# Optimization experiments

Hardware: AMD Instinct MI355X
Metric: run time of the kernel (lower is better)

The kernel has to match this reference:

```python
import jax, jax.numpy as jnp
import numpy as np

D_MODEL, D_STATE, EXPAND, HEADDIM = 768, 64, 2, 64
D_INNER = EXPAND * D_MODEL            # 1536
NHEADS = D_INNER // HEADDIM           # 24
D_IN_PROJ = 2 * D_INNER + 2 * D_STATE + 2 * NHEADS  # 3248
DT_MIN, DT_MAX, DT_INIT_FLOOR, A_FLOOR = 1e-3, 1e-1, 1e-4, 1e-4
LN_EPS = 1e-5


def setup_inputs() -> dict:
    key = jax.random.key(0)
    ks = jax.random.split(key, 8)
    B, L = 2, 1024
    u = jax.random.normal(ks[0], (B, L, D_MODEL), dtype=jnp.float32)
    s_in = 1.0 / np.sqrt(D_MODEL)
    s_out = 1.0 / np.sqrt(D_INNER)
    Win = jax.random.uniform(ks[1], (D_IN_PROJ, D_MODEL), jnp.float32, -s_in, s_in)
    Wout = jax.random.uniform(ks[2], (D_MODEL, D_INNER), jnp.float32, -s_out, s_out)
    _dt = jnp.clip(jnp.exp(jax.random.uniform(ks[3], (NHEADS,)) * (np.log(DT_MAX) - np.log(DT_MIN)) + np.log(DT_MIN)), DT_INIT_FLOOR, None)
    dt_bias = _dt + jnp.log(-jnp.expm1(-_dt))
    D = jnp.ones((NHEADS,), jnp.float32)
    Bg = jnp.ones((D_STATE,), jnp.float32)
    Bb = jnp.zeros((D_STATE,), jnp.float32)
    Cg = jnp.ones((D_STATE,), jnp.float32)
    Cb = jnp.zeros((D_STATE,), jnp.float32)
    return {"u": u, "Win": Win, "Wout": Wout, "dt_bias": dt_bias, "D": D,
            "Bg": Bg, "Bb": Bb, "Cg": Cg, "Cb": Cb}


def _layernorm(x, g, b):
    m = jnp.mean(x, axis=-1, keepdims=True)
    v = jnp.var(x, axis=-1, keepdims=True)
    return (x - m) * jax.lax.rsqrt(v + LN_EPS) * g + b


def reference(u, Win, Wout, dt_bias, D, Bg, Bb, Cg, Cb):
    B_, L, _ = u.shape
    nH, hD, dS = NHEADS, HEADDIM, D_STATE
    proj = u @ Win.T  # (B, L, D_IN_PROJ)
    z, x, Bp, Cp, dd_dt, dd_A = jnp.split(
        proj, np.cumsum([D_INNER, D_INNER, dS, dS, nH])[:-0 or None], axis=-1) if False else (
        proj[..., :D_INNER],
        proj[..., D_INNER:2 * D_INNER],
        proj[..., 2 * D_INNER:2 * D_INNER + dS],
        proj[..., 2 * D_INNER + dS:2 * D_INNER + 2 * dS],
        proj[..., 2 * D_INNER + 2 * dS:2 * D_INNER + 2 * dS + nH],
        proj[..., 2 * D_INNER + 2 * dS + nH:])
    x = x.reshape(B_, L, nH, hD)
    z = z.reshape(B_, L, nH, hD)
    Bn = _layernorm(Bp, Bg, Bb)  # (B, L, dS), shared across heads
    Cn = _layernorm(Cp, Cg, Cb)
    DT = jax.nn.softplus(dd_dt + dt_bias)                    # (B, L, nH)
    A = jnp.minimum(-jax.nn.softplus(dd_A), -A_FLOOR)        # (B, L, nH)
    dec = jnp.exp(A * DT)                                    # (B, L, nH)

    def step(h, inp):
        x_t, Bn_t, Cn_t, DT_t, dec_t = inp
        upd = jnp.einsum('bhp,bn->bhpn', x_t, Bn_t) * DT_t[..., None, None]
        h = dec_t[..., None, None] * h + upd
        y_t = jnp.einsum('bhpn,bn->bhp', h, Cn_t) + D[None, :, None] * x_t
        return h, y_t

    h0 = jnp.zeros((B_, nH, hD, dS), u.dtype)
    xs = (jnp.swapaxes(x, 0, 1), jnp.swapaxes(Bn, 0, 1), jnp.swapaxes(Cn, 0, 1),
          jnp.swapaxes(DT, 0, 1), jnp.swapaxes(dec, 0, 1))
    _, ys = jax.lax.scan(step, h0, xs)            # ys: (L, B, nH, hD)
    y = jnp.swapaxes(ys, 0, 1) * jax.nn.silu(z)   # (B, L, nH, hD)
    y = y.reshape(B_, L, D_INNER)
    return y @ Wout.T
```

## Files before the change

### kernel.cpp

```cpp
#include <hip/hip_runtime.h>
#include <cstdint>

#define D_MODEL   768
#define D_STATE   64
#define D_INNER   1536
#define NHEADS    24
#define HEADDIM   64
#define D_PROJ    3248
#define BATCH     2
#define SEQ       1024
#define ROWS      (BATCH*SEQ)
#define LN_EPS    1e-5f
#define A_FLOOR   1e-4f
#define QC        64
#define NCH       (SEQ/QC)
#define LSTR      72

#define RG_U    32
#define RG_WIN  52
#define RG_WO   12
#define KT_1    24
#define KT_2    48

typedef __attribute__((ext_vector_type(8))) short short8;
typedef __attribute__((ext_vector_type(4))) float f32x4;

__device__ __forceinline__ unsigned short f2bf(float f) {
  union { float f; uint32_t u; } v; v.f = f;
  uint32_t r = (v.u + 0x7FFFu + ((v.u >> 16) & 1u)) >> 16;
  return (unsigned short)r;
}
__device__ __forceinline__ float bf2f(unsigned short u) {
  union { uint32_t u; float f; } v; v.u = (uint32_t)u << 16;
  return v.f;
}
__device__ __forceinline__ void storeC(float v, float* p) { *p = v; }
__device__ __forceinline__ void storeC(float v, unsigned short* p) { *p = f2bf(v); }

__device__ __forceinline__ void gload_lds16(const void* g, void* l) {
  __builtin_amdgcn_global_load_lds(
      (const __attribute__((address_space(1))) unsigned int*)g,
      (__attribute__((address_space(3))) unsigned int*)l, 16, 0, 0);
}

template <int N>
__device__ __forceinline__ void wait_vm() {
  static_assert(N == 0 || N == 2 || N == 3 || N == 4 || N == 6 || N == 8,
                "unsupported vmcnt");
  if constexpr (N == 0) asm volatile("s_waitcnt vmcnt(0)" ::: "memory");
  else if constexpr (N == 2) asm volatile("s_waitcnt vmcnt(2)" ::: "memory");
  else if constexpr (N == 3) asm volatile("s_waitcnt vmcnt(3)" ::: "memory");
  else if constexpr (N == 4) asm volatile("s_waitcnt vmcnt(4)" ::: "memory");
  else if constexpr (N == 6) asm volatile("s_waitcnt vmcnt(6)" ::: "memory");
  else if constexpr (N == 8) asm volatile("s_waitcnt vmcnt(8)" ::: "memory");
}

__global__ __launch_bounds__(256) void pack_all_kernel(
    const float* __restrict__ u, const float* __restrict__ Win,
    const float* __restrict__ Wout, unsigned short* __restrict__ upk,
    unsigned short* __restrict__ Winpk, unsigned short* __restrict__ Wopk) {
  int b = blockIdx.x;
  const float* src; unsigned short* dst; int K, RG, kt, rg, srcRows;
  if (b < KT_1 * RG_U) {
    src = u; dst = upk; K = 768; RG = RG_U; kt = b / RG_U; rg = b % RG_U; srcRows = ROWS;
  } else if (b < KT_1 * RG_U + KT_1 * RG_WIN) {
    int i = b - KT_1 * RG_U;
    src = Win; dst = Winpk; K = 768; RG = RG_WIN; kt = i / RG_WIN; rg = i % RG_WIN; srcRows = D_PROJ;
  } else {
    int i = b - KT_1 * RG_U - KT_1 * RG_WIN;
    src = Wout; dst = Wopk; K = 1536; RG = RG_WO; kt = i / RG_WO; rg = i % RG_WO; srcRows = D_MODEL;
  }
  const int t = threadIdx.x;
  const int lr = t >> 2, cq = t & 3;
  const int R = rg * 64 + lr;
  float4 v0 = make_float4(0.f, 0.f, 0.f, 0.f), v1 = v0;
  if (R < srcRows) {
    const float* p = src + (size_t)R * K + kt * 32 + cq * 8;
    v0 = *(const float4*)p;
    v1 = *(const float4*)(p + 4);
  }
  ushort4 oa, ob;
  oa.x = f2bf(v0.x); oa.y = f2bf(v0.y); oa.z = f2bf(v0.z); oa.w = f2bf(v0.w);
  ob.x = f2bf(v1.x); ob.y = f2bf(v1.y); ob.z = f2bf(v1.z); ob.w = f2bf(v1.w);
  unsigned short* o = dst + ((size_t)(kt * RG + rg) * 4 + cq) * 512 + lr * 8;
  *(ushort4*)o = oa;
  *(ushort4*)(o + 4) = ob;
}

template <int TBM, int TBN, int GX, int GY, bool XMAJOR, typename CT>
__global__ __launch_bounds__(256) void gemm_bt_bf16(
    const unsigned short* __restrict__ A, const unsigned short* __restrict__ B,
    CT* __restrict__ C, int aRG, int bRG, int M, int N, int K) {
  constexpr int MF = TBM / 32;
  constexpr int NF = TBN / 32;
  constexpr int NSA = TBM / 16;
  constexpr int NSB = TBN / 16;
  constexpr int LPW = (NSA + NSB) / 4;
  static_assert((NSA + NSB) % 4 == 0, "segments must split evenly over waves");
  constexpr int NWG = GX * GY;
  constexpr int PER = NWG / 8;
  static_assert(NWG % 8 == 0, "grid must split evenly over 8 XCDs");
  __shared__ unsigned short Asm[4][TBM * 32];
  __shared__ unsigned short Bsm[4][TBN * 32];

  const int tid = threadIdx.x;
  const int wv = tid >> 6, lane = tid & 63;
  const int kTiles = K >> 5;

  const int sk = blockIdx.y;
  A += (size_t)sk * kTiles * aRG * 2048;
  B += (size_t)sk * kTiles * bRG * 2048;
  C += (size_t)sk * M * N;

  const int g = (blockIdx.x & 7) * PER + (blockIdx.x >> 3);
  int bx, by;
  if constexpr (XMAJOR) { by = g / GX; bx = g - by * GX; }
  else                  { bx = g / GY; by = g - bx * GY; }
  const int bm = by * TBM, bn = bx * TBN;

  const int wm = (wv & 1) * (TBM / 2);
  const int wn = (wv >> 1) * (TBN / 2);
  const int gq = lane >> 4, r = lane & 15;

  f32x4 acc[MF][NF];
#pragma unroll
  for (int i = 0; i < MF; ++i)
#pragma unroll
    for (int j = 0; j < NF; ++j) acc[i][j] = (f32x4){0.f, 0.f, 0.f, 0.f};

  auto stage = [&](int kt, int buf) {
    for (int s = wv; s < NSA + NSB; s += 4) {
      if (s < NSA) {
        const unsigned short* src =
            A + ((size_t)kt * aRG + (bm >> 6) + (s >> 2)) * 2048 + (s & 3) * 512 + lane * 8;
        gload_lds16(src, (void*)(&Asm[buf][s * 512]));
      } else {
        int s2 = s - NSA;
        const unsigned short* src =
            B + ((size_t)kt * bRG + (bn >> 6) + (s2 >> 2)) * 2048 + (s2 & 3) * 512 + lane * 8;
        gload_lds16(src, (void*)(&Bsm[buf][s2 * 512]));
      }
    }
  };

  stage(0, 0);
  stage(1, 1);
  stage(2, 2);

  for (int t = 0; t < kTiles; ++t) {
    const int cur = t & 3;
    if (t + 2 < kTiles)      wait_vm<2 * LPW>();
    else if (t + 1 < kTiles) wait_vm<LPW>();
    else                     wait_vm<0>();
    __builtin_amdgcn_s_barrier();
    asm volatile("" ::: "memory");

    if (t + 3 < kTiles) stage(t + 3, (t + 3) & 3);

    short8 a[MF], b[NF];
#pragma unroll
    for (int mf = 0; mf < MF; ++mf) {
      int ra = wm + mf * 16 + r;
      a[mf] = *(const short8*)&Asm[cur][(ra >> 6) * 2048 + gq * 512 + (ra & 63) * 8];
    }
#pragma unroll
    for (int nf = 0; nf < NF; ++nf) {
      int rb = wn + nf * 16 + r;
      b[nf] = *(const short8*)&Bsm[cur][(rb >> 6) * 2048 + gq * 512 + (rb & 63) * 8];
    }
#pragma unroll
    for (int mf = 0; mf < MF; ++mf)
#pragma unroll
      for (int nf = 0; nf < NF; ++nf)
        acc[mf][nf] = __builtin_amdgcn_mfma_f32_16x16x32_bf16(a[mf], b[nf], acc[mf][nf], 0, 0, 0);
  }

#pragma unroll
  for (int mf = 0; mf < MF; ++mf) {
#pragma unroll
    for (int nf = 0; nf < NF; ++nf) {
      int col = bn + wn + nf * 16 + r;
      if (col < N) {
#pragma unroll
        for (int q = 0; q < 4; ++q) {
          int row = bm + wm + mf * 16 + gq * 4 + q;
          storeC(acc[mf][nf][q], &C[(size_t)row * N + col]);
        }
      }
    }
  }
}

__global__ __launch_bounds__(256) void reduce2_kernel(
    const float* __restrict__ P, float* __restrict__ out, int n4) {
  int i = blockIdx.x * 256 + threadIdx.x;
  if (i < n4) {
    float4 a = *(const float4*)(P + (size_t)i * 4);
    float4 b = *(const float4*)(P + (size_t)(n4 + i) * 4);
    a.x += b.x; a.y += b.y; a.z += b.z; a.w += b.w;
    *(float4*)(out + (size_t)i * 4) = a;
  }
}

__device__ __forceinline__ float softplusf(float x) {
  return (x > 20.f) ? x : log1pf(expf(x));
}
__device__ __forceinline__ float wave_sum64(float v) {
#pragma unroll
  for (int o = 32; o > 0; o >>= 1) v += __shfl_xor(v, o);
  return v;
}

__global__ __launch_bounds__(256) void prep_kernel(
    const unsigned short* __restrict__ proj, const float* __restrict__ dt_bias,
    const float* __restrict__ Bg, const float* __restrict__ Bb,
    const float* __restrict__ Cg, const float* __restrict__ Cb,
    unsigned short* __restrict__ BC, float2* __restrict__ aDT) {
  const int r = blockIdx.x * 4 + (threadIdx.x >> 6);
  const int lane = threadIdx.x & 63;
  const unsigned short* p = proj + (size_t)r * D_PROJ;

  float bp = bf2f(p[2 * D_INNER + lane]);
  float cp = bf2f(p[2 * D_INNER + D_STATE + lane]);

  float mb = wave_sum64(bp) * (1.f / 64.f);
  float mc = wave_sum64(cp) * (1.f / 64.f);
  float db = bp - mb, dc = cp - mc;
  float vb = wave_sum64(db * db) * (1.f / 64.f);
  float vc = wave_sum64(dc * dc) * (1.f / 64.f);
  float bn = db * rsqrtf(vb + LN_EPS) * Bg[lane] + Bb[lane];
  float cn = dc * rsqrtf(vc + LN_EPS) * Cg[lane] + Cb[lane];
  BC[(size_t)r * 128 + lane]      = f2bf(bn);
  BC[(size_t)r * 128 + 64 + lane] = f2bf(cn);

  if (lane < NHEADS) {
    float ddt = bf2f(p[2 * D_INNER + 2 * D_STATE + lane]);
    float dA  = bf2f(p[2 * D_INNER + 2 * D_STATE + NHEADS + lane]);
    float DT = softplusf(ddt + dt_bias[lane]);
    float Aa = fminf(-softplusf(dA), -A_FLOOR);
    int b = r >> 10;
    int t = r & 1023;
    aDT[((size_t)(b * NHEADS + lane) << 10) + t] = make_float2(Aa * DT, DT);
  }
}

__device__ __forceinline__ float wave_prefix_incl(float v, int lane) {
#pragma unroll
  for (int o = 1; o < 64; o <<= 1) {
    float w = __shfl_up(v, o);
    if (lane >= o) v += w;
  }
  return v;
}

__global__ __launch_bounds__(256) void chunk_state_kernel(
    const unsigned short* __restrict__ proj, const unsigned short* __restrict__ BC,
    const float2* __restrict__ aDT, float* __restrict__ Tbuf,
    float* __restrict__ Ebuf) {
  const int blk = blockIdx.x;
  const int c = blk & (NCH - 1), bh = blk >> 4;
  const int b = bh / NHEADS, hh = bh % NHEADS;
  const int tid = threadIdx.x;

  __shared__ unsigned short BT[64 * LSTR];
  __shared__ unsigned short XT[64 * LSTR];
  __shared__ float coeff[QC];
  __shared__ float etot[1];

  if (tid < 64) {
    float2 ad = aDT[((size_t)bh << 10) + c * QC + tid];
    float cs = wave_prefix_incl(ad.x, tid);
    float tot = __shfl(cs, 63);
    coeff[tid] = ad.y * __expf(tot - cs);
    if (tid == 63) etot[0] = __expf(tot);
  }
  __syncthreads();

  for (int i = tid; i < 1024; i += 256) {
    int s = i >> 4;
    int q = (i & 15) * 4;
    int r = b * SEQ + c * QC + s;
    ushort4 bv = *(const ushort4*)(BC + (size_t)r * 128 + q);
    ushort4 xv = *(const ushort4*)(proj + (size_t)r * D_PROJ + D_INNER + hh * 64 + q);
    float cf = coeff[s];
    BT[(q + 0) * LSTR + s] = bv.x;
    BT[(q + 1) * LSTR + s] = bv.y;
    BT[(q + 2) * LSTR + s] = bv.z;
    BT[(q + 3) * LSTR + s] = bv.w;
    XT[(q + 0) * LSTR + s] = f2bf(bf2f(xv.x) * cf);
    XT[(q + 1) * LSTR + s] = f2bf(bf2f(xv.y) * cf);
    XT[(q + 2) * LSTR + s] = f2bf(bf2f(xv.z) * cf);
    XT[(q + 3) * LSTR + s] = f2bf(bf2f(xv.w) * cf);
  }
  __syncthreads();

  const int w = tid >> 6, l = tid & 63;
  const int r16 = l & 15, g = l >> 4;
  f32x4 acc[4];
#pragma unroll
  for (int i = 0; i < 4; ++i) acc[i] = (f32x4){0.f, 0.f, 0.f, 0.f};

#pragma unroll
  for (int kk = 0; kk < 2; ++kk) {
    short8 a = *(const short8*)&BT[(w * 16 + r16) * LSTR + kk * 32 + g * 8];
#pragma unroll
    for (int pf = 0; pf < 4; ++pf) {
      short8 bf = *(const short8*)&XT[(pf * 16 + r16) * LSTR + kk * 32 + g * 8];
      acc[pf] = __builtin_amdgcn_mfma_f32_16x16x32_bf16(a, bf, acc[pf], 0, 0, 0);
    }
  }

  float* T = Tbuf + (size_t)blk * 4096;
#pragma unroll
  for (int pf = 0; pf < 4; ++pf)
#pragma unroll
    for (int q = 0; q < 4; ++q)
      T[(size_t)(w * 16 + g * 4 + q) * 64 + pf * 16 + r16] = acc[pf][q];
  if (tid == 0) Ebuf[blk] = etot[0];
}

__global__ __launch_bounds__(256) void interchunk_kernel(
    const float* __restrict__ Tbuf, const float* __restrict__ Ebuf,
    float* __restrict__ Sinbuf) {
  const int bh = blockIdx.x >> 2, part = blockIdx.x & 3;
  const int tid = threadIdx.x;
  const size_t eo = (size_t)part * 1024 + tid * 4;
  float4 s = make_float4(0.f, 0.f, 0.f, 0.f);
#pragma unroll
  for (int c = 0; c < NCH; ++c) {
    size_t off = ((size_t)(bh * NCH + c)) * 4096 + eo;
    *(float4*)(Sinbuf + off) = s;
    float E = Ebuf[bh * NCH + c];
    float4 t4 = *(const float4*)(Tbuf + off);
    s.x = fmaf(E, s.x, t4.x);
    s.y = fmaf(E, s.y, t4.y);
    s.z = fmaf(E, s.z, t4.z);
    s.w = fmaf(E, s.w, t4.w);
  }
}

__global__ __launch_bounds__(256) void chunk_output_kernel(
    const unsigned short* __restrict__ proj, const unsigned short* __restrict__ BC,
    const float2* __restrict__ aDT, const float* __restrict__ Sinbuf,
    const float* __restrict__ Dv, unsigned short* __restrict__ Ybf) {
  const int blk = blockIdx.x;
  const int c = blk & (NCH - 1), bh = blk >> 4;
  const int b = bh / NHEADS, hh = bh % NHEADS;
  const int tid = threadIdx.x;

  __shared__ unsigned short Cc[64 * LSTR];
  __shared__ unsigned short Bc[64 * LSTR];
  __shared__ unsigned short SinT[64 * LSTR];
  __shared__ unsigned short XT[64 * LSTR];
  __shared__ unsigned short Wl[64 * LSTR];
  __shared__ float csum[QC];
  __shared__ float DTs[QC];

  if (tid < 64) {
    float2 ad = aDT[((size_t)bh << 10) + c * QC + tid];
    csum[tid] = wave_prefix_incl(ad.x, tid);
    DTs[tid] = ad.y;
  }

  const size_t sin_base = (size_t)blk * 4096;
  for (int i = tid; i < 1024; i += 256) {
    int s = i >> 4;
    int q = (i & 15) * 4;
    int r = b * SEQ + c * QC + s;
    ushort4 bv = *(const ushort4*)(BC + (size_t)r * 128 + q);
    ushort4 cv = *(const ushort4*)(BC + (size_t)r * 128 + 64 + q);
    ushort4 xv = *(const ushort4*)(proj + (size_t)r * D_PROJ + D_INNER + hh * 64 + q);
    float4 sv = *(const float4*)(Sinbuf + sin_base + (size_t)s * 64 + q);
    *(ushort4*)&Cc[s * LSTR + q] = cv;
    *(ushort4*)&Bc[s * LSTR + q] = bv;
    XT[(q + 0) * LSTR + s] = xv.x;
    XT[(q + 1) * LSTR + s] = xv.y;
    XT[(q + 2) * LSTR + s] = xv.z;
    XT[(q + 3) * LSTR + s] = xv.w;
    SinT[(q + 0) * LSTR + s] = f2bf(sv.x);
    SinT[(q + 1) * LSTR + s] = f2bf(sv.y);
    SinT[(q + 2) * LSTR + s] = f2bf(sv.z);
    SinT[(q + 3) * LSTR + s] = f2bf(sv.w);
  }
  __syncthreads();

  const int w = tid >> 6, l = tid & 63;
  const int r16 = l & 15, g = l >> 4;

  f32x4 accg[4], accy[4];
#pragma unroll
  for (int i = 0; i < 4; ++i) {
    accg[i] = (f32x4){0.f, 0.f, 0.f, 0.f};
    accy[i] = (f32x4){0.f, 0.f, 0.f, 0.f};
  }

#pragma unroll
  for (int kk = 0; kk < 2; ++kk) {
    short8 a = *(const short8*)&Cc[(w * 16 + r16) * LSTR + kk * 32 + g * 8];
#pragma unroll
    for (int f = 0; f < 4; ++f) {
      short8 bf = *(const short8*)&Bc[(f * 16 + r16) * LSTR + kk * 32 + g * 8];
      accg[f] = __builtin_amdgcn_mfma_f32_16x16x32_bf16(a, bf, accg[f], 0, 0, 0);
    }
#pragma unroll
    for (int f = 0; f < 4; ++f) {
      short8 bf = *(const short8*)&SinT[(f * 16 + r16) * LSTR + kk * 32 + g * 8];
      accy[f] = __builtin_amdgcn_mfma_f32_16x16x32_bf16(a, bf, accy[f], 0, 0, 0);
    }
  }

  float cst[4], dsc[4];
#pragma unroll
  for (int q = 0; q < 4; ++q) {
    cst[q] = csum[w * 16 + g * 4 + q];
    dsc[q] = __expf(cst[q]);
  }
#pragma unroll
  for (int sf = 0; sf < 4; ++sf) {
    int s = sf * 16 + r16;
    float cs_s = csum[s], dt_s = DTs[s];
#pragma unroll
    for (int q = 0; q < 4; ++q) {
      int t = w * 16 + g * 4 + q;
      float wv = (s <= t) ? accg[sf][q] * __expf(cst[q] - cs_s) * dt_s : 0.f;
      Wl[t * LSTR + s] = f2bf(wv);
    }
  }
#pragma unroll
  for (int f = 0; f < 4; ++f)
#pragma unroll
    for (int q = 0; q < 4; ++q) accy[f][q] *= dsc[q];
  __syncthreads();

#pragma unroll
  for (int kk = 0; kk < 2; ++kk) {
    short8 a = *(const short8*)&Wl[(w * 16 + r16) * LSTR + kk * 32 + g * 8];
#pragma unroll
    for (int f = 0; f < 4; ++f) {
      short8 bf = *(const short8*)&XT[(f * 16 + r16) * LSTR + kk * 32 + g * 8];
      accy[f] = __builtin_amdgcn_mfma_f32_16x16x32_bf16(a, bf, accy[f], 0, 0, 0);
    }
  }

  const float Dh = Dv[hh];
  const int rg = b * 16 + c;
#pragma unroll
  for (int pf = 0; pf < 4; ++pf) {
    int p = pf * 16 + r16;
    int col = hh * 64 + p;
    int kt = col >> 5;
    int cseg = (col >> 3) & 3;
    int jj = p & 7;
    size_t base = ((size_t)(kt * RG_U + rg) * 4 + cseg) * 512 + jj;
#pragma unroll
    for (int q = 0; q < 4; ++q) {
      int t = w * 16 + g * 4 + q;
      int rr = b * SEQ + c * QC + t;
      float x = bf2f(proj[(size_t)rr * D_PROJ + D_INNER + hh * 64 + p]);
      float z = bf2f(proj[(size_t)rr * D_PROJ + hh * 64 + p]);
      float y = accy[pf][q] + Dh * x;
      Ybf[base + (size_t)t * 8] = f2bf(y * (z / (1.f + __expf(-z))));
    }
  }
}

extern "C" void kernel_launch(void* const* d_in, const int* in_sizes, int n_in,
                              void* d_out, int out_size, void* d_ws, size_t ws_size,
                              hipStream_t stream) {
  const float* u       = (const float*)d_in[0];
  const float* Win     = (const float*)d_in[1];
  const float* Wout    = (const float*)d_in[2];
  const float* dt_bias = (const float*)d_in[3];
  const float* Dv      = (const float*)d_in[4];
  const float* Bg      = (const float*)d_in[5];
  const float* Bb      = (const float*)d_in[6];
  const float* Cg      = (const float*)d_in[7];
  const float* Cb      = (const float*)d_in[8];
  float* out = (float*)d_out;

  float* ws = (float*)d_ws;
  unsigned short* projsh = (unsigned short*)ws;
  float*  after_proj = ws + (size_t)ROWS * D_PROJ / 2;
  unsigned short* BCsh = (unsigned short*)after_proj;
  float*  aDTf    = after_proj + (size_t)ROWS * 128 / 2;
  float2* aDT     = (float2*)aDTf;
  float*  Tbuf    = aDTf + (size_t)2 * BATCH * NHEADS * SEQ;
  float*  Ebuf    = Tbuf + (size_t)BATCH * NHEADS * NCH * 4096;
  float*  Sinbuf  = Ebuf + 1024;
  float*  Woutbff = Sinbuf + (size_t)BATCH * NHEADS * NCH * 4096;
  float*  Pbuf    = Woutbff + 589824;

  unsigned short* upk   = (unsigned short*)Sinbuf;
  unsigned short* Winpk = (unsigned short*)Tbuf;
  unsigned short* Ypk   = (unsigned short*)Tbuf;
  unsigned short* Wopk  = (unsigned short*)Woutbff;

  pack_all_kernel<<<KT_1 * RG_U + KT_1 * RG_WIN + KT_2 * RG_WO, 256, 0, stream>>>(
      u, Win, Wout, upk, Winpk, Wopk);

  gemm_bt_bf16<128, 128, 26, 16, false><<<416, 256, 0, stream>>>(
      upk, Winpk, projsh, RG_U, RG_WIN, ROWS, D_PROJ, D_MODEL);

  prep_kernel<<<ROWS / 4, 256, 0, stream>>>(projsh, dt_bias, Bg, Bb, Cg, Cb, BCsh, aDT);

  chunk_state_kernel<<<BATCH * NHEADS * NCH, 256, 0, stream>>>(projsh, BCsh, aDT, Tbuf, Ebuf);
  interchunk_kernel<<<BATCH * NHEADS * 4, 256, 0, stream>>>(Tbuf, Ebuf, Sinbuf);
  chunk_output_kernel<<<BATCH * NHEADS * NCH, 256, 0, stream>>>(projsh, BCsh, aDT, Sinbuf, Dv, Ypk);

  gemm_bt_bf16<64, 64, 12, 32, true><<<dim3(384, 2), 256, 0, stream>>>(
      Ypk, Wopk, Pbuf, RG_U, RG_WO, ROWS, D_MODEL, D_INNER / 2);
  reduce2_kernel<<<1536, 256, 0, stream>>>(Pbuf, out, ROWS * D_MODEL / 4);
}
```

Baseline: 81.42 us.

## Replace split-K grid and reduce kernel with intra-block K split via LDS reduction

The output GEMM previously ran split-K across a second grid dimension, wrote fp32 partials to a workspace, and summed them in a separate reduce kernel. Now each block has 512 threads; the two groups of four waves each process half of K in separate LDS buffers and combine partials through LDS before storing directly to the output. The pipeline depth also drops from four to three stage buffers to fit the doubled LDS footprint. This removes one kernel launch and a round trip of the partial buffer through global memory, at the cost of halving block count and larger per-block LDS use.

```diff
diff --git a/kernel.cpp b/kernel.cpp
--- a/kernel.cpp
+++ b/kernel.cpp
@@ -87,8 +87,8 @@
   *(ushort4*)(o + 4) = ob;
 }
 
-template <int TBM, int TBN, int GX, int GY, bool XMAJOR, typename CT>
-__global__ __launch_bounds__(256) void gemm_bt_bf16(
+template <int TBM, int TBN, int GX, int GY, bool XMAJOR, int SPLIT, typename CT>
+__global__ __launch_bounds__(256 * SPLIT) void gemm_bt_bf16(
     const unsigned short* __restrict__ A, const unsigned short* __restrict__ B,
     CT* __restrict__ C, int aRG, int bRG, int M, int N, int K) {
   constexpr int MF = TBM / 32;
@@ -100,17 +100,15 @@
   constexpr int NWG = GX * GY;
   constexpr int PER = NWG / 8;
   static_assert(NWG % 8 == 0, "grid must split evenly over 8 XCDs");
-  __shared__ unsigned short Asm[4][TBM * 32];
-  __shared__ unsigned short Bsm[4][TBN * 32];
+  __shared__ unsigned short Asm[SPLIT][3][TBM * 32];
+  __shared__ unsigned short Bsm[SPLIT][3][TBN * 32];
 
   const int tid = threadIdx.x;
-  const int wv = tid >> 6, lane = tid & 63;
-  const int kTiles = K >> 5;
-
-  const int sk = blockIdx.y;
-  A += (size_t)sk * kTiles * aRG * 2048;
-  B += (size_t)sk * kTiles * bRG * 2048;
-  C += (size_t)sk * M * N;
+  const int w = tid >> 6, lane = tid & 63;
+  const int khalf = w >> 2;
+  const int wv = w & 3;
+  const int kTiles = (K / SPLIT) >> 5;
+  const int ktBase = khalf * kTiles;
 
   const int g = (blockIdx.x & 7) * PER + (blockIdx.x >> 3);
   int bx, by;
@@ -128,51 +126,75 @@
 #pragma unroll
     for (int j = 0; j < NF; ++j) acc[i][j] = (f32x4){0.f, 0.f, 0.f, 0.f};
 
-  auto stage = [&](int kt, int buf) {
+  auto stage = [&](int t, int buf) {
+    const int kt = ktBase + t;
     for (int s = wv; s < NSA + NSB; s += 4) {
       if (s < NSA) {
         const unsigned short* src =
             A + ((size_t)kt * aRG + (bm >> 6) + (s >> 2)) * 2048 + (s & 3) * 512 + lane * 8;
-        gload_lds16(src, (void*)(&Asm[buf][s * 512]));
+        gload_lds16(src, (void*)(&Asm[khalf][buf][s * 512]));
       } else {
         int s2 = s - NSA;
         const unsigned short* src =
             B + ((size_t)kt * bRG + (bn >> 6) + (s2 >> 2)) * 2048 + (s2 & 3) * 512 + lane * 8;
-        gload_lds16(src, (void*)(&Bsm[buf][s2 * 512]));
+        gload_lds16(src, (void*)(&Bsm[khalf][buf][s2 * 512]));
       }
     }
   };
 
   stage(0, 0);
   stage(1, 1);
-  stage(2, 2);
-
+
+  int cur = 0;
   for (int t = 0; t < kTiles; ++t) {
-    const int cur = t & 3;
-    if (t + 2 < kTiles)      wait_vm<2 * LPW>();
-    else if (t + 1 < kTiles) wait_vm<LPW>();
-    else                     wait_vm<0>();
+    if (t + 1 < kTiles) wait_vm<LPW>();
+    else                wait_vm<0>();
     __builtin_amdgcn_s_barrier();
     asm volatile("" ::: "memory");
 
-    if (t + 3 < kTiles) stage(t + 3, (t + 3) & 3);
+    if (t + 2 < kTiles) stage(t + 2, (t + 2) % 3);
 
     short8 a[MF], b[NF];
 #pragma unroll
     for (int mf = 0; mf < MF; ++mf) {
       int ra = wm + mf * 16 + r;
-      a[mf] = *(const short8*)&Asm[cur][(ra >> 6) * 2048 + gq * 512 + (ra & 63) * 8];
+      a[mf] = *(const short8*)&Asm[khalf][cur][(ra >> 6) * 2048 + gq * 512 + (ra & 63) * 8];
     }
 #pragma unroll
     for (int nf = 0; nf < NF; ++nf) {
       int rb = wn + nf * 16 + r;
-      b[nf] = *(const short8*)&Bsm[cur][(rb >> 6) * 2048 + gq * 512 + (rb & 63) * 8];
+      b[nf] = *(const short8*)&Bsm[khalf][cur][(rb >> 6) * 2048 + gq * 512 + (rb & 63) * 8];
     }
 #pragma unroll
     for (int mf = 0; mf < MF; ++mf)
 #pragma unroll
       for (int nf = 0; nf < NF; ++nf)
         acc[mf][nf] = __builtin_amdgcn_mfma_f32_16x16x32_bf16(a[mf], b[nf], acc[mf][nf], 0, 0, 0);
+
+    cur = (cur + 1) % 3;
+  }
+
+  if constexpr (SPLIT == 2) {
+    __syncthreads();
+    float* red = (float*)&Asm[0][0][0];
+    if (khalf == 1) {
+#pragma unroll
+      for (int mf = 0; mf < MF; ++mf)
+#pragma unroll
+        for (int nf = 0; nf < NF; ++nf)
+#pragma unroll
+          for (int q = 0; q < 4; ++q)
+            red[(size_t)wv * 1024 + ((mf * NF + nf) * 4 + q) * 64 + lane] = acc[mf][nf][q];
+    }
+    __syncthreads();
+    if (khalf == 1) return;
+#pragma unroll
+    for (int mf = 0; mf < MF; ++mf)
+#pragma unroll
+      for (int nf = 0; nf < NF; ++nf)
+#pragma unroll
+        for (int q = 0; q < 4; ++q)
+          acc[mf][nf][q] += red[(size_t)wv * 1024 + ((mf * NF + nf) * 4 + q) * 64 + lane];
   }
 
 #pragma unroll
@@ -188,17 +210,6 @@
         }
       }
     }
-  }
-}
-
-__global__ __launch_bounds__(256) void reduce2_kernel(
-    const float* __restrict__ P, float* __restrict__ out, int n4) {
-  int i = blockIdx.x * 256 + threadIdx.x;
-  if (i < n4) {
-    float4 a = *(const float4*)(P + (size_t)i * 4);
-    float4 b = *(const float4*)(P + (size_t)(n4 + i) * 4);
-    a.x += b.x; a.y += b.y; a.z += b.z; a.w += b.w;
-    *(float4*)(out + (size_t)i * 4) = a;
   }
 }
 
@@ -488,7 +499,6 @@
   float*  Ebuf    = Tbuf + (size_t)BATCH * NHEADS * NCH * 4096;
   float*  Sinbuf  = Ebuf + 1024;
   float*  Woutbff = Sinbuf + (size_t)BATCH * NHEADS * NCH * 4096;
-  float*  Pbuf    = Woutbff + 589824;
 
   unsigned short* upk   = (unsigned short*)Sinbuf;
   unsigned short* Winpk = (unsigned short*)Tbuf;
@@ -498,7 +508,7 @@
   pack_all_kernel<<<KT_1 * RG_U + KT_1 * RG_WIN + KT_2 * RG_WO, 256, 0, stream>>>(
       u, Win, Wout, upk, Winpk, Wopk);
 
-  gemm_bt_bf16<128, 128, 26, 16, false><<<416, 256, 0, stream>>>(
+  gemm_bt_bf16<128, 128, 26, 16, false, 1, unsigned short><<<416, 256, 0, stream>>>(
       upk, Winpk, projsh, RG_U, RG_WIN, ROWS, D_PROJ, D_MODEL);
 
   prep_kernel<<<ROWS / 4, 256, 0, stream>>>(projsh, dt_bias, Bg, Bb, Cg, Cb, BCsh, aDT);
@@ -507,7 +517,6 @@
   interchunk_kernel<<<BATCH * NHEADS * 4, 256, 0, stream>>>(Tbuf, Ebuf, Sinbuf);
   chunk_output_kernel<<<BATCH * NHEADS * NCH, 256, 0, stream>>>(projsh, BCsh, aDT, Sinbuf, Dv, Ypk);
 
-  gemm_bt_bf16<64, 64, 12, 32, true><<<dim3(384, 2), 256, 0, stream>>>(
-      Ypk, Wopk, Pbuf, RG_U, RG_WO, ROWS, D_MODEL, D_INNER / 2);
-  reduce2_kernel<<<1536, 256, 0, stream>>>(Pbuf, out, ROWS * D_MODEL / 4);
-}
+  gemm_bt_bf16<64, 64, 12, 32, true, 2, float><<<384, 512, 0, stream>>>(
+      Ypk, Wopk, out, RG_U, RG_WO, ROWS, D_MODEL, D_INNER);
+}
```

Result: faster. 78.57 us, median of 2 (-3.5%).
